# Optimization experiments

Hardware: AMD Instinct MI355X
Metric: run time of the kernel (lower is better)

The kernel has to match this reference:

```python
import jax, jax.numpy as jnp
import numpy as np

B, S, D, Q = 2, 2048, 2048, 16
H = D // Q  # head dim = 128


def _precompute_mask(s):
    # additive causal mask: -1e9 strictly above the diagonal
    m = jnp.full((s, s), -1000000000.0, dtype=jnp.float32)
    return jnp.triu(m, k=1)


def _precompute_rope(head, s):
    # inv_freq over even indices 0,2,...,head-2
    inv_freq = 1.0 / (10000.0 ** (jnp.arange(0, head, 2, dtype=jnp.float32) / head))  # [H/2]
    freqs = jnp.arange(s, dtype=jnp.float32)[:, None] * inv_freq[None, :]  # [S, H/2]
    emb = jnp.concatenate([freqs, freqs], axis=-1)  # [S, H]
    return jnp.sin(emb), jnp.cos(emb)


def _rotate_half(x):
    x1, x2 = jnp.split(x, 2, axis=-1)
    return jnp.concatenate([-x2, x1], axis=-1)


def _apply_rope(x, sin, cos):
    # x: [B, Q, S, H]; sin/cos: [S, H] broadcast over batch & heads
    return x * cos + _rotate_half(x) * sin


def setup_inputs() -> dict:
    key = jax.random.key(0)
    kx, kq, kk, kv, ko = jax.random.split(key, 5)
    wscale = 1.0 / np.sqrt(D)
    x = jax.random.normal(kx, (B, S, D), dtype=jnp.float32)
    wq = jax.random.normal(kq, (D, D), dtype=jnp.float32) * wscale
    wk = jax.random.normal(kk, (D, D), dtype=jnp.float32) * wscale
    wv = jax.random.normal(kv, (D, D), dtype=jnp.float32) * wscale
    wo = jax.random.normal(ko, (D, D), dtype=jnp.float32) * wscale
    mask = _precompute_mask(S)
    sin, cos = _precompute_rope(H, S)
    return {"x": x, "wq": wq, "wk": wk, "wv": wv, "wo": wo,
            "mask": mask, "sin": sin, "cos": cos}


def reference(x, wq, wk, wv, wo, mask, sin, cos):
    b, s, d = x.shape
    # projections: [B,S,D] @ [D, Q*H] -> [B,S,Q,H] -> [B,Q,S,H]
    def proj(w):
        t = jnp.einsum('bsd,de->bse', x, w).reshape(b, s, Q, H)
        return t.transpose(0, 2, 1, 3)
    q, k, v = proj(wq), proj(wk), proj(wv)
    q = _apply_rope(q, sin, cos)
    k = _apply_rope(k, sin, cos) * (H ** -0.5)
    # scores [B,Q,S,Skv] + causal mask, softmax over kv
    a = jnp.einsum('bqsh,bqth->bqst', q, k) + mask
    a = jax.nn.softmax(a, axis=-1)
    y = jnp.einsum('bqst,bqth->bqsh', a, v)  # [B,Q,S,H]
    y = y.transpose(0, 2, 1, 3).reshape(b, s, Q * H)  # [B,S,D]
    return jnp.einsum('bsd,de->bse', y, wo)
```

## Files before the change

### kernel.cpp

```cpp
#include <hip/hip_runtime.h>

typedef unsigned short u16;
typedef unsigned int u32;
typedef __attribute__((ext_vector_type(8))) short bf16x8;
typedef __attribute__((ext_vector_type(4))) float f32x4;
typedef __bf16 bf16v8 __attribute__((ext_vector_type(8)));

__device__ __forceinline__ u16 f2bf(float x) {
  u32 u = __float_as_uint(x);
  u32 r = (u + 0x7FFFu + ((u >> 16) & 1u)) >> 16;
  return (u16)r;
}
__device__ __forceinline__ float bf2f(u16 x) { return __uint_as_float(((u32)x) << 16); }

__device__ __forceinline__ void mfma_bf16(f32x4& d, bf16x8 a, bf16x8 b) {
  d = __builtin_amdgcn_mfma_f32_16x16x32_bf16(
        __builtin_bit_cast(bf16v8, a), __builtin_bit_cast(bf16v8, b), d, 0, 0, 0);
}

__device__ __forceinline__ void gload16(const u16* g, u16* l) {
  __builtin_amdgcn_global_load_lds((const __attribute__((address_space(1))) u32*)g,
                                   (__attribute__((address_space(3))) u32*)l, 16, 0, 0);
}

__device__ __forceinline__ void store_c(u16* p, float v) { *p = f2bf(v); }
__device__ __forceinline__ void store_c(float* p, float v) { *p = v; }

__global__ void cvt4(const float* __restrict__ in, u16* __restrict__ out, int n4) {
  int i = blockIdx.x * 256 + threadIdx.x;
  if (i >= n4) return;
  float4 v = reinterpret_cast<const float4*>(in)[i];
  u32 lo = (u32)f2bf(v.x) | ((u32)f2bf(v.y) << 16);
  u32 hi = (u32)f2bf(v.z) | ((u32)f2bf(v.w) << 16);
  reinterpret_cast<uint2*>(out)[i] = make_uint2(lo, hi);
}

__global__ void wtrans3(const float* __restrict__ wq, const float* __restrict__ wk,
                        const float* __restrict__ wv,
                        u16* __restrict__ wqkt, u16* __restrict__ wvt) {
  const float* in; u16* out;
  switch (blockIdx.z) {
    case 0: in = wq; out = wqkt; break;
    case 1: in = wk; out = wqkt + (size_t)2048 * 2048; break;
    default: in = wv; out = wvt; break;
  }
  __shared__ float t[32][33];
  int n0 = blockIdx.x * 32, k0 = blockIdx.y * 32;
  int tx = threadIdx.x, ty = threadIdx.y;
#pragma unroll
  for (int j = 0; j < 4; ++j)
    t[ty + 8 * j][tx] = in[(size_t)(k0 + ty + 8 * j) * 2048 + n0 + tx];
  __syncthreads();
#pragma unroll
  for (int j = 0; j < 4; ++j)
    out[(size_t)(n0 + ty + 8 * j) * 2048 + k0 + tx] = f2bf(t[tx][ty + 8 * j]);
}

__global__ void wtrans1(const float* __restrict__ in, u16* __restrict__ out) {
  __shared__ float t[32][33];
  int n0 = blockIdx.x * 32, k0 = blockIdx.y * 32;
  int tx = threadIdx.x, ty = threadIdx.y;
#pragma unroll
  for (int j = 0; j < 4; ++j)
    t[ty + 8 * j][tx] = in[(size_t)(k0 + ty + 8 * j) * 2048 + n0 + tx];
  __syncthreads();
#pragma unroll
  for (int j = 0; j < 4; ++j)
    out[(size_t)(n0 + ty + 8 * j) * 2048 + k0 + tx] = f2bf(t[tx][ty + 8 * j]);
}

template <int BM, int BN, int WM, int WN, typename CT>
__global__ __launch_bounds__(512, 2) void gemm256t(const u16* __restrict__ A,
                                                   const u16* __restrict__ Bt,
                                                   CT* __restrict__ C,
                                                   int M, int N, int K) {
  constexpr int MR = BM / WM / 16;
  constexpr int NR = BN / WN / 16;
  constexpr int CH = (BM + BN) / 128;
  __shared__ u16 lds[2][(BM + BN) * 32];
  int tid = threadIdx.x;
  int lane = tid & 63, wave = tid >> 6;
  int g = lane >> 4, lr = lane & 15;
  int wr = wave / WN, wc = wave % WN;
  size_t brow = (size_t)blockIdx.y * BM, bcol = (size_t)blockIdx.x * BN;

  auto stage = [&](int kt, int bf) {
#pragma unroll
    for (int i = 0; i < CH; ++i) {
      int c = i * 512 + tid;
      bool isA = c < BM * 4;
      int p = isA ? c : c - BM * 4;
      int row = p >> 2, pc = p & 3;
      int lc = pc ^ ((row >> 1) & 3);
      const u16* src = isA ? A  + (brow + row) * (size_t)K + kt + lc * 8
                           : Bt + (bcol + row) * (size_t)K + kt + lc * 8;
      gload16(src, &lds[bf][(isA ? 0 : BM * 32) + p * 8]);
    }
  };

  f32x4 acc[MR][NR];
#pragma unroll
  for (int m = 0; m < MR; ++m)
#pragma unroll
    for (int n = 0; n < NR; ++n) acc[m][n] = (f32x4){0.f, 0.f, 0.f, 0.f};

  int NT = K >> 5;
  stage(0, 0);
  stage(32, 1);
  for (int t = 0; t < NT; ++t) {
    if (t == NT - 1) asm volatile("s_waitcnt vmcnt(0)" ::: "memory");
    else             asm volatile("s_waitcnt vmcnt(%0)" :: "i"(CH) : "memory");
    __builtin_amdgcn_s_barrier();
    int bf = t & 1;
    const u16* La = &lds[bf][0];
    const u16* Lb = &lds[bf][BM * 32];
    __builtin_amdgcn_s_setprio(1);
    bf16x8 bfr[NR];
#pragma unroll
    for (int n = 0; n < NR; ++n) {
      int colr = wc * (BN / WN) + n * 16 + lr;
      bfr[n] = *(const bf16x8*)&Lb[colr * 32 + ((g ^ ((colr >> 1) & 3)) * 8)];
    }
#pragma unroll
    for (int m = 0; m < MR; ++m) {
      int rowr = wr * (BM / WM) + m * 16 + lr;
      bf16x8 afr = *(const bf16x8*)&La[rowr * 32 + ((g ^ ((rowr >> 1) & 3)) * 8)];
#pragma unroll
      for (int n = 0; n < NR; ++n) mfma_bf16(acc[m][n], afr, bfr[n]);
    }
    __builtin_amdgcn_s_setprio(0);
    __builtin_amdgcn_s_barrier();
    if (t + 2 < NT) stage((t + 2) * 32, bf);
  }
#pragma unroll
  for (int m = 0; m < MR; ++m)
#pragma unroll
    for (int n = 0; n < NR; ++n) {
      size_t row = brow + wr * (BM / WM) + m * 16 + 4 * g;
      size_t col = bcol + wc * (BN / WN) + n * 16 + lr;
#pragma unroll
      for (int r = 0; r < 4; ++r) store_c(&C[(row + r) * (size_t)N + col], acc[m][n][r]);
    }
}

__global__ void rope_kernel(u16* __restrict__ qk,
                            const float* __restrict__ sn, const float* __restrict__ cs) {
  int idx = blockIdx.x * 256 + threadIdx.x;
  int d = idx & 63;
  int h = (idx >> 6) & 15;
  int bs = idx >> 10;
  int s = bs & 2047;
  size_t base = ((size_t)bs << 12) + h * 128;
  float c1 = cs[s * 128 + d], c2 = cs[s * 128 + d + 64];
  float s1 = sn[s * 128 + d], s2 = sn[s * 128 + d + 64];
  float q1 = bf2f(qk[base + d]), q2 = bf2f(qk[base + d + 64]);
  float k1 = bf2f(qk[base + 2048 + d]), k2 = bf2f(qk[base + 2048 + d + 64]);
  qk[base + d]      = f2bf(q1 * c1 - q2 * s1);
  qk[base + d + 64] = f2bf(q2 * c2 + q1 * s2);
  const float ks = 0.08838834764831845f;
  qk[base + 2048 + d]      = f2bf((k1 * c1 - k2 * s1) * ks);
  qk[base + 2048 + d + 64] = f2bf((k2 * c2 + k1 * s2) * ks);
}

__global__ __launch_bounds__(512, 2) void attn(const u16* __restrict__ qk,
                                               const u16* __restrict__ vt,
                                               u16* __restrict__ y) {
  __shared__ u16 Ks[3][64 * 128];
  __shared__ u16 Vs[3][128 * 64];
  __shared__ u32 P_lds[8][16][33];
  int tid = threadIdx.x;
  int wave = tid >> 6, lane = tid & 63;
  int g = lane >> 4, lr = lane & 15;
  int b = blockIdx.z, h = blockIdx.y, bx = blockIdx.x;

  const u16* Q  = qk + ((size_t)b * 2048) * 4096 + h * 128;
  const u16* K  = qk + ((size_t)b * 2048) * 4096 + 2048 + h * 128;
  const u16* Vg = vt + (size_t)h * 128 * 4096 + (size_t)b * 2048;
  u16* Y = y + ((size_t)b * 2048) * 2048 + h * 128;

  auto stage = [&](int kv0, int bf) {
#pragma unroll
    for (int i = 0; i < 2; ++i) {
      int c = tid + 512 * i;
      int krow = c >> 4, kphys = (c & 15) << 4;
      gload16(K + (size_t)(kv0 + krow) * 4096 + ((kphys ^ ((krow & 7) << 4)) >> 1),
              &Ks[bf][c * 8]);
      int vrow = c >> 3, vphys = c & 7;
      gload16(Vg + (size_t)vrow * 4096 + kv0 + ((vphys ^ (vrow & 7)) * 8),
              &Vs[bf][c * 8]);
    }
  };

  for (int seg = 0; seg < 2; ++seg) {
    int sup = seg ? (15 - bx) : bx;
    int ntiles = 2 * sup + 2;
    int q0w = sup * 128 + wave * 16;

    bf16x8 qfr[4];
#pragma unroll
    for (int dc = 0; dc < 4; ++dc)
      qfr[dc] = *(const bf16x8*)&Q[(size_t)(q0w + lr) * 4096 + dc * 32 + g * 8];

    f32x4 o[8];
#pragma unroll
    for (int i = 0; i < 8; ++i) o[i] = (f32x4){0.f, 0.f, 0.f, 0.f};
    float lsum = 0.f;

    __syncthreads();
    stage(0, 0);
    stage(64, 1);
    if (ntiles > 2) stage(128, 2);
    int buf = 0;
    for (int t = 0; t < ntiles; ++t) {
      int w = ntiles - 1 - t;
      if (w >= 2)      asm volatile("s_waitcnt vmcnt(8)" ::: "memory");
      else if (w == 1) asm volatile("s_waitcnt vmcnt(4)" ::: "memory");
      else             asm volatile("s_waitcnt vmcnt(0)" ::: "memory");
      __builtin_amdgcn_s_barrier();
      int kv0 = t * 64;
      f32x4 st[4];
#pragma unroll
      for (int n = 0; n < 4; ++n) {
        f32x4 s4 = (f32x4){0.f, 0.f, 0.f, 0.f};
        int row = n * 16 + lr;
#pragma unroll
        for (int dc = 0; dc < 4; ++dc) {
          bf16x8 kfr = *(const bf16x8*)
              &Ks[buf][row * 128 + (((dc * 64 + 16 * g) ^ ((row & 7) << 4)) >> 1)];
          mfma_bf16(s4, kfr, qfr[dc]);
        }
        st[n] = s4;
      }
      int qg = q0w + lr;
      u32 pk[8];
#pragma unroll
      for (int n = 0; n < 4; ++n)
#pragma unroll
        for (int rp = 0; rp < 2; ++rp) {
          int kvb = kv0 + n * 16 + 4 * g + rp * 2;
          float p0 = (kvb     <= qg) ? __expf(st[n][rp * 2])     : 0.f;
          float p1 = (kvb + 1 <= qg) ? __expf(st[n][rp * 2 + 1]) : 0.f;
          lsum += p0 + p1;
          pk[n * 2 + rp] = (u32)f2bf(p0) | ((u32)f2bf(p1) << 16);
        }
#pragma unroll
      for (int n = 0; n < 4; ++n) {
        P_lds[wave][lr][8 * n + 2 * g]     = pk[n * 2];
        P_lds[wave][lr][8 * n + 2 * g + 1] = pk[n * 2 + 1];
      }
      asm volatile("" ::: "memory");
#pragma unroll
      for (int kh = 0; kh < 2; ++kh) {
        union { u32 w[4]; bf16x8 v; } pu;
#pragma unroll
        for (int j = 0; j < 4; ++j)
          pu.w[j] = P_lds[wave][lr][16 * kh + 4 * g + j];
        bf16x8 pf = pu.v;
#pragma unroll
        for (int dch = 0; dch < 8; ++dch) {
          int vr = dch * 16 + lr;
          bf16x8 vfr = *(const bf16x8*)
              &Vs[buf][vr * 64 + (((4 * kh + g) ^ (lr & 7)) * 8)];
          mfma_bf16(o[dch], pf, vfr);
        }
      }
      __builtin_amdgcn_s_barrier();
      if (t + 3 < ntiles) stage((t + 3) * 64, buf);
      buf = (buf == 2) ? 0 : buf + 1;
    }
    lsum += __shfl_xor(lsum, 16);
    lsum += __shfl_xor(lsum, 32);
    float linv[4];
#pragma unroll
    for (int r = 0; r < 4; ++r) linv[r] = 1.f / __shfl(lsum, 4 * g + r);
#pragma unroll
    for (int dch = 0; dch < 8; ++dch)
#pragma unroll
      for (int r = 0; r < 4; ++r)
        Y[(size_t)(q0w + 4 * g + r) * 2048 + dch * 16 + lr] = f2bf(o[dch][r] * linv[r]);
  }
}

extern "C" void kernel_launch(void* const* d_in, const int* in_sizes, int n_in,
                              void* d_out, int out_size, void* d_ws, size_t ws_size,
                              hipStream_t stream) {
  const float* x  = (const float*)d_in[0];
  const float* wq = (const float*)d_in[1];
  const float* wk = (const float*)d_in[2];
  const float* wv = (const float*)d_in[3];
  const float* wo = (const float*)d_in[4];
  const float* sn = (const float*)d_in[6];
  const float* cs = (const float*)d_in[7];

  char* W = (char*)d_ws;
  u16* xb   = (u16*)(W);
  u16* wqkt = (u16*)(W + (size_t)16 * 1024 * 1024);
  u16* wvt  = (u16*)(W + (size_t)32 * 1024 * 1024);
  u16* vt   = (u16*)(W + (size_t)40 * 1024 * 1024);
  u16* qkb  = (u16*)d_out;
  u16* yb   = xb;

  dim3 tb(32, 8);
  cvt4<<<8192, 256, 0, stream>>>(x, xb, 2097152);
  wtrans3<<<dim3(64, 64, 3), tb, 0, stream>>>(wq, wk, wv, wqkt, wvt);
  gemm256t<256, 256, 2, 4, u16><<<dim3(16, 16), 512, 0, stream>>>(
      xb, wqkt, qkb, 4096, 4096, 2048);
  gemm256t<256, 128, 4, 2, u16><<<dim3(32, 8), 512, 0, stream>>>(
      wvt, xb, vt, 2048, 4096, 2048);
  wtrans1<<<dim3(64, 64), tb, 0, stream>>>(wo, wvt);
  rope_kernel<<<16384, 256, 0, stream>>>(qkb, sn, cs);
  attn<<<dim3(8, 16, 2), 512, 0, stream>>>(qkb, vt, yb);
  gemm256t<128, 256, 2, 4, float><<<dim3(8, 32), 512, 0, stream>>>(
      yb, wvt, (float*)d_out, 4096, 2048, 2048);
}
```

Measured before the change: 274.5 us.

## Give each attention wave two query subtiles, halve block size, double-buffer K/V

```diff
diff --git a/kernel.cpp b/kernel.cpp
--- a/kernel.cpp
+++ b/kernel.cpp
@@ -162,12 +162,12 @@
   qk[base + 2048 + d + 64] = f2bf((k2 * c2 + k1 * s2) * ks);
 }
 
-__global__ __launch_bounds__(512, 2) void attn(const u16* __restrict__ qk,
+__global__ __launch_bounds__(256, 2) void attn(const u16* __restrict__ qk,
                                                const u16* __restrict__ vt,
                                                u16* __restrict__ y) {
-  __shared__ u16 Ks[3][64 * 128];
-  __shared__ u16 Vs[3][128 * 64];
-  __shared__ u32 P_lds[8][16][33];
+  __shared__ u16 Ks[2][64 * 128];
+  __shared__ u16 Vs[2][128 * 64];
+  __shared__ u32 P_lds[4][32 * 32];
   int tid = threadIdx.x;
   int wave = tid >> 6, lane = tid & 63;
   int g = lane >> 4, lr = lane & 15;
@@ -180,104 +180,122 @@
 
   auto stage = [&](int kv0, int bf) {
 #pragma unroll
-    for (int i = 0; i < 2; ++i) {
-      int c = tid + 512 * i;
+    for (int i = 0; i < 4; ++i) {
+      int c = tid + 256 * i;
       int krow = c >> 4, kphys = (c & 15) << 4;
       gload16(K + (size_t)(kv0 + krow) * 4096 + ((kphys ^ ((krow & 7) << 4)) >> 1),
               &Ks[bf][c * 8]);
+    }
+#pragma unroll
+    for (int i = 0; i < 4; ++i) {
+      int c = tid + 256 * i;
       int vrow = c >> 3, vphys = c & 7;
       gload16(Vg + (size_t)vrow * 4096 + kv0 + ((vphys ^ (vrow & 7)) * 8),
               &Vs[bf][c * 8]);
     }
   };
 
+  auto pidx = [](int row, int c) { return row * 32 + ((c + 2 * row) & 31); };
+
   for (int seg = 0; seg < 2; ++seg) {
     int sup = seg ? (15 - bx) : bx;
     int ntiles = 2 * sup + 2;
-    int q0w = sup * 128 + wave * 16;
-
-    bf16x8 qfr[4];
-#pragma unroll
-    for (int dc = 0; dc < 4; ++dc)
-      qfr[dc] = *(const bf16x8*)&Q[(size_t)(q0w + lr) * 4096 + dc * 32 + g * 8];
-
-    f32x4 o[8];
-#pragma unroll
-    for (int i = 0; i < 8; ++i) o[i] = (f32x4){0.f, 0.f, 0.f, 0.f};
-    float lsum = 0.f;
+    int q0w = sup * 128 + wave * 32;
+
+    bf16x8 qfr[2][4];
+#pragma unroll
+    for (int qg2 = 0; qg2 < 2; ++qg2)
+#pragma unroll
+      for (int dc = 0; dc < 4; ++dc)
+        qfr[qg2][dc] = *(const bf16x8*)
+            &Q[(size_t)(q0w + qg2 * 16 + lr) * 4096 + dc * 32 + g * 8];
+
+    f32x4 o0[8], o1[8];
+#pragma unroll
+    for (int i = 0; i < 8; ++i) { o0[i] = (f32x4){0,0,0,0}; o1[i] = (f32x4){0,0,0,0}; }
+    float ls0 = 0.f, ls1 = 0.f;
 
     __syncthreads();
     stage(0, 0);
     stage(64, 1);
-    if (ntiles > 2) stage(128, 2);
-    int buf = 0;
     for (int t = 0; t < ntiles; ++t) {
-      int w = ntiles - 1 - t;
-      if (w >= 2)      asm volatile("s_waitcnt vmcnt(8)" ::: "memory");
-      else if (w == 1) asm volatile("s_waitcnt vmcnt(4)" ::: "memory");
-      else             asm volatile("s_waitcnt vmcnt(0)" ::: "memory");
+      if (t + 1 < ntiles) asm volatile("s_waitcnt vmcnt(8)" ::: "memory");
+      else                asm volatile("s_waitcnt vmcnt(0)" ::: "memory");
       __builtin_amdgcn_s_barrier();
-      int kv0 = t * 64;
-      f32x4 st[4];
+      int kv0 = t * 64, buf = t & 1;
+      f32x4 st0[4], st1[4];
 #pragma unroll
       for (int n = 0; n < 4; ++n) {
-        f32x4 s4 = (f32x4){0.f, 0.f, 0.f, 0.f};
+        f32x4 s0 = (f32x4){0,0,0,0}, s1 = (f32x4){0,0,0,0};
         int row = n * 16 + lr;
 #pragma unroll
         for (int dc = 0; dc < 4; ++dc) {
           bf16x8 kfr = *(const bf16x8*)
               &Ks[buf][row * 128 + (((dc * 64 + 16 * g) ^ ((row & 7) << 4)) >> 1)];
-          mfma_bf16(s4, kfr, qfr[dc]);
+          mfma_bf16(s0, kfr, qfr[0][dc]);
+          mfma_bf16(s1, kfr, qfr[1][dc]);
         }
-        st[n] = s4;
+        st0[n] = s0; st1[n] = s1;
       }
-      int qg = q0w + lr;
-      u32 pk[8];
+      int qa = q0w + lr, qb = q0w + 16 + lr;
+      u32 pk0[8], pk1[8];
 #pragma unroll
       for (int n = 0; n < 4; ++n)
 #pragma unroll
         for (int rp = 0; rp < 2; ++rp) {
           int kvb = kv0 + n * 16 + 4 * g + rp * 2;
-          float p0 = (kvb     <= qg) ? __expf(st[n][rp * 2])     : 0.f;
-          float p1 = (kvb + 1 <= qg) ? __expf(st[n][rp * 2 + 1]) : 0.f;
-          lsum += p0 + p1;
-          pk[n * 2 + rp] = (u32)f2bf(p0) | ((u32)f2bf(p1) << 16);
+          float a0 = (kvb     <= qa) ? __expf(st0[n][rp * 2])     : 0.f;
+          float a1 = (kvb + 1 <= qa) ? __expf(st0[n][rp * 2 + 1]) : 0.f;
+          ls0 += a0 + a1;
+          pk0[n * 2 + rp] = (u32)f2bf(a0) | ((u32)f2bf(a1) << 16);
+          float b0 = (kvb     <= qb) ? __expf(st1[n][rp * 2])     : 0.f;
+          float b1 = (kvb + 1 <= qb) ? __expf(st1[n][rp * 2 + 1]) : 0.f;
+          ls1 += b0 + b1;
+          pk1[n * 2 + rp] = (u32)f2bf(b0) | ((u32)f2bf(b1) << 16);
         }
 #pragma unroll
       for (int n = 0; n < 4; ++n) {
-        P_lds[wave][lr][8 * n + 2 * g]     = pk[n * 2];
-        P_lds[wave][lr][8 * n + 2 * g + 1] = pk[n * 2 + 1];
+        *(uint2*)&P_lds[wave][pidx(lr,      8 * n + 2 * g)] = make_uint2(pk0[2 * n], pk0[2 * n + 1]);
+        *(uint2*)&P_lds[wave][pidx(16 + lr, 8 * n + 2 * g)] = make_uint2(pk1[2 * n], pk1[2 * n + 1]);
       }
       asm volatile("" ::: "memory");
 #pragma unroll
       for (int kh = 0; kh < 2; ++kh) {
-        union { u32 w[4]; bf16x8 v; } pu;
-#pragma unroll
-        for (int j = 0; j < 4; ++j)
-          pu.w[j] = P_lds[wave][lr][16 * kh + 4 * g + j];
-        bf16x8 pf = pu.v;
+        union { u32 w[4]; bf16x8 v; } pu0, pu1;
+#pragma unroll
+        for (int j = 0; j < 4; ++j) {
+          pu0.w[j] = P_lds[wave][pidx(lr,      16 * kh + 4 * g + j)];
+          pu1.w[j] = P_lds[wave][pidx(16 + lr, 16 * kh + 4 * g + j)];
+        }
+        bf16x8 pf0 = pu0.v, pf1 = pu1.v;
 #pragma unroll
         for (int dch = 0; dch < 8; ++dch) {
           int vr = dch * 16 + lr;
           bf16x8 vfr = *(const bf16x8*)
               &Vs[buf][vr * 64 + (((4 * kh + g) ^ (lr & 7)) * 8)];
-          mfma_bf16(o[dch], pf, vfr);
+          mfma_bf16(o0[dch], pf0, vfr);
+          mfma_bf16(o1[dch], pf1, vfr);
         }
       }
+      asm volatile("" ::: "memory");
       __builtin_amdgcn_s_barrier();
-      if (t + 3 < ntiles) stage((t + 3) * 64, buf);
-      buf = (buf == 2) ? 0 : buf + 1;
-    }
-    lsum += __shfl_xor(lsum, 16);
-    lsum += __shfl_xor(lsum, 32);
-    float linv[4];
-#pragma unroll
-    for (int r = 0; r < 4; ++r) linv[r] = 1.f / __shfl(lsum, 4 * g + r);
+      if (t + 2 < ntiles) stage((t + 2) * 64, buf);
+    }
+    ls0 += __shfl_xor(ls0, 16); ls0 += __shfl_xor(ls0, 32);
+    ls1 += __shfl_xor(ls1, 16); ls1 += __shfl_xor(ls1, 32);
+    float li0[4], li1[4];
+#pragma unroll
+    for (int r = 0; r < 4; ++r) {
+      li0[r] = 1.f / __shfl(ls0, 4 * g + r);
+      li1[r] = 1.f / __shfl(ls1, 4 * g + r);
+    }
 #pragma unroll
     for (int dch = 0; dch < 8; ++dch)
 #pragma unroll
-      for (int r = 0; r < 4; ++r)
-        Y[(size_t)(q0w + 4 * g + r) * 2048 + dch * 16 + lr] = f2bf(o[dch][r] * linv[r]);
+      for (int r = 0; r < 4; ++r) {
+        Y[(size_t)(q0w + 4 * g + r) * 2048 + dch * 16 + lr]      = f2bf(o0[dch][r] * li0[r]);
+        Y[(size_t)(q0w + 16 + 4 * g + r) * 2048 + dch * 16 + lr] = f2bf(o1[dch][r] * li1[r]);
+      }
   }
 }
 
@@ -309,7 +327,7 @@
       wvt, xb, vt, 2048, 4096, 2048);
   wtrans1<<<dim3(64, 64), tb, 0, stream>>>(wo, wvt);
   rope_kernel<<<16384, 256, 0, stream>>>(qkb, sn, cs);
-  attn<<<dim3(8, 16, 2), 512, 0, stream>>>(qkb, vt, yb);
+  attn<<<dim3(8, 16, 2), 256, 0, stream>>>(qkb, vt, yb);
   gemm256t<128, 256, 2, 4, float><<<dim3(8, 32), 512, 0, stream>>>(
       yb, wvt, (float*)d_out, 4096, 2048, 2048);
 }
```

Measured after the change: 281.7 us, median of 2. +2.6%, slower.
